# Kernel tuning notes

Measured on AMD Instinct MI355X. Metric: run time of the kernel, lower is better.

Reference implementation:

```python
import jax, jax.numpy as jnp
import numpy as np

N_NODES = 50000
N_EDGES = 800000
DIMS = [128, 512, 256, 128]
EPS = 1e-5


def setup_inputs() -> dict:
    key = jax.random.key(0)
    ks = jax.random.split(key, 2 + 5 * 3)
    inp = {
        "x": jax.random.normal(ks[0], (N_NODES, DIMS[0]), dtype=jnp.float32),
        "edge_index": jax.random.randint(ks[1], (2, N_EDGES), 0, N_NODES, dtype=jnp.int64),
    }
    ki = 2
    for i in range(3):
        din, dout = DIMS[i], DIMS[i + 1]
        s = 1.0 / np.sqrt(din)
        inp[f"Wl{i}"] = jax.random.uniform(ks[ki + 0], (din, dout), jnp.float32, -s, s)
        inp[f"bl{i}"] = jax.random.uniform(ks[ki + 1], (dout,), jnp.float32, -s, s)
        inp[f"Wr{i}"] = jax.random.uniform(ks[ki + 2], (din, dout), jnp.float32, -s, s)
        inp[f"g{i}"] = jnp.ones((dout,), jnp.float32)
        inp[f"b{i}"] = jnp.zeros((dout,), jnp.float32)
        ki += 5
    return inp


def _sage_mean(x, src, dst, Wl, bl, Wr):
    n = x.shape[0]
    agg = jax.ops.segment_sum(x[src], dst, num_segments=n)  # [N, din]
    deg = jax.ops.segment_sum(jnp.ones((src.shape[0],), x.dtype), dst, num_segments=n)
    mean = agg / jnp.maximum(deg, 1.0)[:, None]
    return mean @ Wl + bl + x @ Wr


def _bn(h, gamma, beta):
    m = h.mean(axis=0)
    v = h.var(axis=0)
    return gamma * (h - m) * jax.lax.rsqrt(v + EPS) + beta


def reference(x, edge_index, Wl0, bl0, Wr0, g0, b0, Wl1, bl1, Wr1, g1, b1, Wl2, bl2, Wr2, g2, b2):
    src, dst = edge_index[0], edge_index[1]
    params = [(Wl0, bl0, Wr0, g0, b0), (Wl1, bl1, Wr1, g1, b1), (Wl2, bl2, Wr2, g2, b2)]
    h = x
    for Wl, bl, Wr, g, b in params:
        h = _sage_mean(h, src, dst, Wl, bl, Wr)
        h = _bn(h, g, b)
        h = jax.nn.relu(h)
        # dropout: identity in eval mode
    return h
```

## Files before the change

kernel.cpp:

```cpp
#include <hip/hip_runtime.h>
#include <cstdint>
#include <cstddef>


#define EPS_BN 1e-5f

typedef unsigned short ushort_t;
typedef __attribute__((ext_vector_type(8))) short short8;
typedef __attribute__((ext_vector_type(4))) float float4v;

__device__ __forceinline__ float bf2f(ushort_t u) {
    union { unsigned int i; float f; } v; v.i = ((unsigned int)u) << 16; return v.f;
}
__device__ __forceinline__ ushort_t f2bf(float f) {
    union { float f; unsigned int i; } v; v.f = f;
    unsigned int r = v.i + 0x7fffu + ((v.i >> 16) & 1u);
    return (ushort_t)(r >> 16);
}

__device__ __forceinline__ void async_copy16(void* lds, const void* g) {
    __builtin_amdgcn_global_load_lds(
        (const __attribute__((address_space(1))) unsigned int*)g,
        (__attribute__((address_space(3))) unsigned int*)lds, 16, 0, 0);
}

__global__ void detect_fmt_kernel(const int* __restrict__ edges, int* __restrict__ nz) {
    int t = threadIdx.x;
    int cnt = 0;
    #pragma unroll
    for (int j = 0; j < 4; ++j) {
        int idx = 2 * (t * 4 + j) + 1;
        if (edges[idx] != 0) cnt++;
    }
    if (cnt) atomicAdd(nz, cnt);
}

__device__ __forceinline__ void edge_sd(const int* __restrict__ p, int e, int ne,
                                        bool is64, int& s, int& d) {
    if (is64) { s = p[2 * e];  d = p[2 * ne + 2 * e]; }
    else      { s = p[e];      d = p[ne + e]; }
}

__global__ void count_deg_kernel(const int* __restrict__ edges, int ne,
                                 const int* __restrict__ nz, int* __restrict__ degi) {
    bool is64 = (*nz == 0);
    int e = blockIdx.x * 256 + threadIdx.x;
    if (e < ne) {
        int s, d; edge_sd(edges, e, ne, is64, s, d);
        atomicAdd(&degi[d], 1);
    }
}

__global__ void scan1_kernel(const int* __restrict__ degi, int n,
                             int* __restrict__ rowptr, int* __restrict__ bsums) {
    __shared__ int sh[1024];
    int t = threadIdx.x;
    int i = blockIdx.x * 1024 + t;
    int v = (i < n) ? degi[i] : 0;
    sh[t] = v;
    __syncthreads();
    for (int off = 1; off < 1024; off <<= 1) {
        int x = (t >= off) ? sh[t - off] : 0;
        __syncthreads();
        sh[t] += x;
        __syncthreads();
    }
    if (i < n) rowptr[i] = sh[t] - v;
    if (t == 1023) bsums[blockIdx.x] = sh[t];
}

__global__ void scan2_kernel(int* __restrict__ bsums, int nb,
                             int* __restrict__ rowptr, int n, int total) {
    if (threadIdx.x == 0 && blockIdx.x == 0) {
        int run = 0;
        for (int b = 0; b < nb; ++b) { int t = bsums[b]; bsums[b] = run; run += t; }
        rowptr[n] = total;
    }
}

__global__ void scan3_kernel(int* __restrict__ rowptr, int n,
                             const int* __restrict__ bsums, int* __restrict__ cursor) {
    int i = blockIdx.x * 1024 + threadIdx.x;
    if (i < n) {
        int v = rowptr[i] + bsums[blockIdx.x];
        rowptr[i] = v;
        cursor[i] = v;
    }
}

__global__ void scatter_kernel(const int* __restrict__ edges, int ne,
                               const int* __restrict__ nz,
                               int* __restrict__ cursor, int* __restrict__ csr_src) {
    bool is64 = (*nz == 0);
    int e = blockIdx.x * 256 + threadIdx.x;
    if (e < ne) {
        int s, d; edge_sd(edges, e, ne, is64, s, d);
        int pos = atomicAdd(&cursor[d], 1);
        csr_src[pos] = s;
    }
}

__global__ void f2b_kernel(const float* __restrict__ in, ushort_t* __restrict__ out, int n) {
    int i = blockIdx.x * 256 + threadIdx.x;
    if (i < n) out[i] = f2bf(in[i]);
}

__global__ void prep_wt_kernel(const float* __restrict__ Wl, const float* __restrict__ Wr,
                               ushort_t* __restrict__ WT, int K1, int Dout) {
    int idx = blockIdx.x * 256 + threadIdx.x;
    int K2 = 2 * K1;
    if (idx >= Dout * K2) return;
    int n = idx / K2, k = idx - n * K2;
    float v = (k < K1) ? Wl[(size_t)k * Dout + n] : Wr[(size_t)(k - K1) * Dout + n];
    WT[idx] = f2bf(v);
}

__global__ void prep_wtc_kernel(const float* __restrict__ Wl, const float* __restrict__ Wr,
                                ushort_t* __restrict__ WTc, int K, int D) {
    int idx = blockIdx.x * 256 + threadIdx.x;
    if (idx >= 2 * D * K) return;
    int nn = idx / K, k = idx - nn * K;
    float v = (nn < D) ? Wl[(size_t)k * D + nn] : Wr[(size_t)k * D + (nn - D)];
    WTc[idx] = f2bf(v);
}

template <int VEC> struct VecT;
template <> struct VecT<2> { using T = unsigned int; };
template <> struct VecT<4> { using T = uint2; };
template <> struct VecT<8> { using T = uint4; };

template <int VEC>
__device__ __forceinline__ void vunpack(typename VecT<VEC>::T v, unsigned int* w) {
    if constexpr (VEC == 2) { w[0] = v; }
    else if constexpr (VEC == 4) { w[0] = v.x; w[1] = v.y; }
    else { w[0] = v.x; w[1] = v.y; w[2] = v.z; w[3] = v.w; }
}

template <int VEC>
__device__ __forceinline__ void vaccum(typename VecT<VEC>::T v, float* acc) {
    unsigned int w[VEC / 2];
    vunpack<VEC>(v, w);
    #pragma unroll
    for (int i = 0; i < VEC / 2; ++i) {
        acc[2 * i + 0] += bf2f((ushort_t)(w[i] & 0xffffu));
        acc[2 * i + 1] += bf2f((ushort_t)(w[i] >> 16));
    }
}

template <int VEC>
__global__ __launch_bounds__(256) void aggregate_wave_kernel(
    const ushort_t* __restrict__ h, ushort_t* __restrict__ mean,
    const int* __restrict__ rowptr, const int* __restrict__ csr_src, int nnodes) {
    const int din = VEC * 64;
    int wid = blockIdx.x * 4 + (threadIdx.x >> 6);
    if (wid >= nnodes) return;
    int lane = threadIdx.x & 63;
    int e0 = rowptr[wid], e1 = rowptr[wid + 1];
    const ushort_t* base = h + (size_t)lane * VEC;

    float acc[VEC];
    #pragma unroll
    for (int i = 0; i < VEC; ++i) acc[i] = 0.f;

    using VT = typename VecT<VEC>::T;
    int e = e0;
    for (; e + 4 <= e1; e += 4) {
        int s0 = csr_src[e], s1 = csr_src[e + 1], s2 = csr_src[e + 2], s3 = csr_src[e + 3];
        VT v0 = *(const VT*)(base + (size_t)s0 * din);
        VT v1 = *(const VT*)(base + (size_t)s1 * din);
        VT v2 = *(const VT*)(base + (size_t)s2 * din);
        VT v3 = *(const VT*)(base + (size_t)s3 * din);
        vaccum<VEC>(v0, acc); vaccum<VEC>(v1, acc);
        vaccum<VEC>(v2, acc); vaccum<VEC>(v3, acc);
    }
    for (; e < e1; ++e) {
        int s = csr_src[e];
        vaccum<VEC>(*(const VT*)(base + (size_t)s * din), acc);
    }

    int deg = e1 - e0;
    float scale = 1.0f / (float)(deg > 1 ? deg : 1);
    unsigned int o[VEC / 2];
    #pragma unroll
    for (int i = 0; i < VEC / 2; ++i)
        o[i] = (unsigned int)f2bf(acc[2 * i] * scale) |
               ((unsigned int)f2bf(acc[2 * i + 1] * scale) << 16);
    VT ov;
    if constexpr (VEC == 2) { ov = o[0]; }
    else if constexpr (VEC == 4) { ov.x = o[0]; ov.y = o[1]; }
    else { ov.x = o[0]; ov.y = o[1]; ov.z = o[2]; ov.w = o[3]; }
    *(VT*)(mean + (size_t)wid * din + (size_t)lane * VEC) = ov;
}

template <int VEC>
__global__ __launch_bounds__(256) void aggregate_add_kernel(
    const ushort_t* __restrict__ PR, const float* __restrict__ bias,
    float* __restrict__ outf,
    const int* __restrict__ rowptr, const int* __restrict__ csr_src, int nnodes) {
    const int D = VEC * 64;
    const int stride = 2 * D;
    int wid = blockIdx.x * 4 + (threadIdx.x >> 6);
    if (wid >= nnodes) return;
    int lane = threadIdx.x & 63;
    int e0 = rowptr[wid], e1 = rowptr[wid + 1];
    const ushort_t* base = PR + (size_t)lane * VEC;

    float acc[VEC];
    #pragma unroll
    for (int i = 0; i < VEC; ++i) acc[i] = 0.f;

    using VT = typename VecT<VEC>::T;
    int e = e0;
    for (; e + 4 <= e1; e += 4) {
        int s0 = csr_src[e], s1 = csr_src[e + 1], s2 = csr_src[e + 2], s3 = csr_src[e + 3];
        VT v0 = *(const VT*)(base + (size_t)s0 * stride);
        VT v1 = *(const VT*)(base + (size_t)s1 * stride);
        VT v2 = *(const VT*)(base + (size_t)s2 * stride);
        VT v3 = *(const VT*)(base + (size_t)s3 * stride);
        vaccum<VEC>(v0, acc); vaccum<VEC>(v1, acc);
        vaccum<VEC>(v2, acc); vaccum<VEC>(v3, acc);
    }
    for (; e < e1; ++e) {
        int s = csr_src[e];
        vaccum<VEC>(*(const VT*)(base + (size_t)s * stride), acc);
    }

    int deg = e1 - e0;
    float scale = 1.0f / (float)(deg > 1 ? deg : 1);

    VT rv = *(const VT*)(PR + (size_t)wid * stride + D + (size_t)lane * VEC);
    unsigned int rw[VEC / 2];
    vunpack<VEC>(rv, rw);
    float o[VEC];
    #pragma unroll
    for (int i = 0; i < VEC / 2; ++i) {
        o[2 * i + 0] = bf2f((ushort_t)(rw[i] & 0xffffu));
        o[2 * i + 1] = bf2f((ushort_t)(rw[i] >> 16));
    }
    #pragma unroll
    for (int i = 0; i < VEC; ++i)
        o[i] += acc[i] * scale + bias[lane * VEC + i];
    #pragma unroll
    for (int i = 0; i < VEC; ++i)
        outf[(size_t)wid * D + lane * VEC + i] = o[i];
}

template <bool DUAL, bool BF16OUT>
__global__ __launch_bounds__(256) void gemm_glds_kernel(
    const ushort_t* __restrict__ A1, const ushort_t* __restrict__ A2,
    const ushort_t* __restrict__ BT, const float* __restrict__ bias,
    float* __restrict__ Cf, ushort_t* __restrict__ Cb,
    int N, int K1, int Ktot, int Wtot) {
    __shared__ ushort_t As[128 * 32];
    __shared__ ushort_t Bs[128 * 32];

    const int tid = threadIdx.x;
    const int wave = tid >> 6;
    const int lane = tid & 63;
    const int quad = lane >> 4;
    const int l15 = lane & 15;
    const int rowBase = blockIdx.y * 128;
    const int colBase = blockIdx.x * 128;
    const int wm = (wave >> 1) * 64;
    const int wn = (wave & 1) * 64;

    float4v acc[4][4];
    #pragma unroll
    for (int i = 0; i < 4; ++i)
        #pragma unroll
        for (int j = 0; j < 4; ++j)
            acc[i][j] = (float4v){0.f, 0.f, 0.f, 0.f};

    const int nkt = Ktot / 32;
    const int khalf = K1 / 32;

    for (int kt = 0; kt < nkt; ++kt) {
        const ushort_t* Asrc = A1;
        int kg = kt * 32;
        if (DUAL && kt >= khalf) { Asrc = A2; kg = (kt - khalf) * 32; }
        const int kb = kt * 32;

        #pragma unroll
        for (int u = 0; u < 2; ++u) {
            int c = u * 256 + tid;
            int r = c >> 2, off = (c & 3) * 8;
            int grow = rowBase + r;
            if (grow >= N) grow = N - 1;
            async_copy16(&As[c * 8], Asrc + (size_t)grow * K1 + kg + off);
            async_copy16(&Bs[c * 8], BT + (size_t)(colBase + r) * Ktot + kb + off);
        }
        __syncthreads();

        short8 af[4], bf4[4];
        #pragma unroll
        for (int i = 0; i < 4; ++i)
            af[i] = *(const short8*)&As[(wm + i * 16 + l15) * 32 + quad * 8];
        #pragma unroll
        for (int j = 0; j < 4; ++j)
            bf4[j] = *(const short8*)&Bs[(wn + j * 16 + l15) * 32 + quad * 8];

        #pragma unroll
        for (int i = 0; i < 4; ++i)
            #pragma unroll
            for (int j = 0; j < 4; ++j)
                acc[i][j] = __builtin_amdgcn_mfma_f32_16x16x32_bf16(bf4[j], af[i], acc[i][j], 0, 0, 0);
        __syncthreads();
    }

    if (BF16OUT) {
        ushort_t* lws = (wave < 2) ? &As[wave * 2048] : &Bs[(wave - 2) * 2048];
        #pragma unroll
        for (int p = 0; p < 2; ++p) {
            #pragma unroll
            for (int jj = 0; jj < 2; ++jj) {
                int j = 2 * p + jj;
                #pragma unroll
                for (int i = 0; i < 4; ++i) {
                    uint2 pk;
                    pk.x = (unsigned int)f2bf(acc[i][j][0]) | ((unsigned int)f2bf(acc[i][j][1]) << 16);
                    pk.y = (unsigned int)f2bf(acc[i][j][2]) | ((unsigned int)f2bf(acc[i][j][3]) << 16);
                    *(uint2*)&lws[(i * 16 + l15) * 32 + jj * 16 + quad * 4] = pk;
                }
            }
            __syncthreads();
            #pragma unroll
            for (int it = 0; it < 4; ++it) {
                int c = it * 64 + lane;
                int row = c >> 2, coff = (c & 3) * 8;
                int grow = rowBase + wm + row;
                if (grow < N) {
                    uint4 v = *(const uint4*)&lws[row * 32 + coff];
                    *(uint4*)(Cb + (size_t)grow * Wtot + colBase + wn + p * 32 + coff) = v;
                }
            }
            __syncthreads();
        }
    } else {
        float* lwf = (float*)((wave < 2) ? (void*)&As[wave * 2048] : (void*)&Bs[(wave - 2) * 2048]);
        #pragma unroll
        for (int j = 0; j < 4; ++j) {
            int colb = colBase + wn + j * 16 + quad * 4;
            float4 bv = *(const float4*)(bias + colb);
            #pragma unroll
            for (int i = 0; i < 4; ++i) {
                float4 o;
                o.x = acc[i][j][0] + bv.x;
                o.y = acc[i][j][1] + bv.y;
                o.z = acc[i][j][2] + bv.z;
                o.w = acc[i][j][3] + bv.w;
                *(float4*)&lwf[(i * 16 + l15) * 16 + quad * 4] = o;
            }
            __syncthreads();
            #pragma unroll
            for (int it = 0; it < 4; ++it) {
                int c = it * 64 + lane;
                int row = c >> 2, coff = (c & 3) * 4;
                int grow = rowBase + wm + row;
                if (grow < N)
                    *(float4*)(Cf + (size_t)grow * Wtot + colBase + wn + j * 16 + coff) =
                        *(const float4*)&lwf[row * 16 + coff];
            }
            __syncthreads();
        }
    }
}

__global__ void colstats_kernel(const float* __restrict__ h, int N, int D,
                                float* __restrict__ sum, float* __restrict__ sumsq) {
    int col = blockIdx.x * 64 + (threadIdx.x & 63);
    int lane = threadIdx.x >> 6;
    float s = 0.f, s2 = 0.f;
    int stride = gridDim.y * 4;
    for (int r = blockIdx.y * 4 + lane; r < N; r += stride) {
        float v = h[(size_t)r * D + col];
        s += v;
        s2 += v * v;
    }
    atomicAdd(&sum[col], s);
    atomicAdd(&sumsq[col], s2);
}

__global__ void bn_relu_bf16_kernel(const float* __restrict__ h, ushort_t* __restrict__ hb,
                                    int N, int D,
                                    const float* __restrict__ sum, const float* __restrict__ sumsq,
                                    const float* __restrict__ g, const float* __restrict__ b) {
    size_t idx = (size_t)blockIdx.x * blockDim.x + threadIdx.x;
    if (idx >= (size_t)N * D) return;
    int col = (int)(idx & (size_t)(D - 1));
    float m = sum[col] / (float)N;
    float var = sumsq[col] / (float)N - m * m;
    float inv = rsqrtf(var + EPS_BN);
    float v = h[idx];
    v = g[col] * (v - m) * inv + b[col];
    hb[idx] = f2bf(v > 0.f ? v : 0.f);
}

__global__ void bn_relu_kernel(float* __restrict__ h, int N, int D,
                               const float* __restrict__ sum, const float* __restrict__ sumsq,
                               const float* __restrict__ g, const float* __restrict__ b) {
    size_t idx = (size_t)blockIdx.x * blockDim.x + threadIdx.x;
    if (idx >= (size_t)N * D) return;
    int col = (int)(idx & (size_t)(D - 1));
    float m = sum[col] / (float)N;
    float var = sumsq[col] / (float)N - m * m;
    float inv = rsqrtf(var + EPS_BN);
    float v = h[idx];
    v = g[col] * (v - m) * inv + b[col];
    h[idx] = v > 0.f ? v : 0.f;
}

extern "C" void kernel_launch(void* const* d_in, const int* in_sizes, int n_in,
                              void* d_out, int out_size, void* d_ws, size_t ws_size,
                              hipStream_t stream) {
    const float* x     = (const float*)d_in[0];
    const int*   edges = (const int*)d_in[1];
    const float* Wl0 = (const float*)d_in[2];
    const float* bl0 = (const float*)d_in[3];
    const float* Wr0 = (const float*)d_in[4];
    const float* g0  = (const float*)d_in[5];
    const float* b0  = (const float*)d_in[6];
    const float* Wl1 = (const float*)d_in[7];
    const float* bl1 = (const float*)d_in[8];
    const float* Wr1 = (const float*)d_in[9];
    const float* g1  = (const float*)d_in[10];
    const float* b1  = (const float*)d_in[11];
    const float* Wl2 = (const float*)d_in[12];
    const float* bl2 = (const float*)d_in[13];
    const float* Wr2 = (const float*)d_in[14];
    const float* g2  = (const float*)d_in[15];
    const float* b2  = (const float*)d_in[16];

    const int D0 = 128, D1 = 512, D2 = 256, D3 = 128;
    const int n  = in_sizes[0] / D0;
    const int ne = in_sizes[1] / 2;

    char* base = (char*)d_ws;
    size_t off = 0;
    auto alloc = [&](size_t bytes) -> char* {
        char* p = base + off;
        off = (off + bytes + 255) & ~(size_t)255;
        return p;
    };
    int*      nzflag  = (int*)alloc(4);
    int*      degi    = (int*)alloc((size_t)n * 4);
    int*      rowptr  = (int*)alloc((size_t)(n + 1) * 4);
    int*      cursor  = (int*)alloc((size_t)n * 4);
    int*      csr_src = (int*)alloc((size_t)ne * 4);
    int*      bsums   = (int*)alloc(64 * 4);
    float*    stats   = (float*)alloc(6 * 512 * 4);
    ushort_t* xb      = (ushort_t*)alloc((size_t)n * D0 * 2);
    ushort_t* mb      = (ushort_t*)alloc((size_t)n * 512 * 2);
    ushort_t* h1b     = (ushort_t*)alloc((size_t)n * D1 * 2);
    ushort_t* h2b     = (ushort_t*)alloc((size_t)n * D2 * 2);
    float*    hf      = (float*)alloc((size_t)n * 512 * 4);
    ushort_t* WT0     = (ushort_t*)alloc((size_t)D1 * 2 * D0 * 2);
    ushort_t* WT1c    = (ushort_t*)alloc((size_t)(2 * D2) * D1 * 2);
    ushort_t* WT2c    = (ushort_t*)alloc((size_t)(2 * D3) * D2 * 2);
    float*    out     = (float*)d_out;
    (void)ws_size; (void)n_in; (void)out_size;

    hipMemsetAsync(nzflag, 0, 4, stream);
    hipMemsetAsync(degi, 0, (size_t)n * 4, stream);
    hipMemsetAsync(stats, 0, 6 * 512 * 4, stream);

    detect_fmt_kernel<<<1, 256, 0, stream>>>(edges, nzflag);
    count_deg_kernel<<<(ne + 255) / 256, 256, 0, stream>>>(edges, ne, nzflag, degi);
    int nscan = (n + 1023) / 1024;
    scan1_kernel<<<nscan, 1024, 0, stream>>>(degi, n, rowptr, bsums);
    scan2_kernel<<<1, 64, 0, stream>>>(bsums, nscan, rowptr, n, ne);
    scan3_kernel<<<nscan, 1024, 0, stream>>>(rowptr, n, bsums, cursor);
    scatter_kernel<<<(ne + 255) / 256, 256, 0, stream>>>(edges, ne, nzflag, cursor, csr_src);

    f2b_kernel<<<((size_t)n * D0 + 255) / 256, 256, 0, stream>>>(x, xb, n * D0);
    prep_wt_kernel<<<(D1 * 2 * D0 + 255) / 256, 256, 0, stream>>>(Wl0, Wr0, WT0, D0, D1);
    prep_wtc_kernel<<<(2 * D2 * D1 + 255) / 256, 256, 0, stream>>>(Wl1, Wr1, WT1c, D1, D2);
    prep_wtc_kernel<<<(2 * D3 * D2 + 255) / 256, 256, 0, stream>>>(Wl2, Wr2, WT2c, D2, D3);

    const int aggGrid = (n + 3) / 4;
    const int rowBlocks = (n + 127) / 128;

    aggregate_wave_kernel<2><<<aggGrid, 256, 0, stream>>>(xb, mb, rowptr, csr_src, n);
    gemm_glds_kernel<true, false><<<dim3(D1 / 128, rowBlocks), 256, 0, stream>>>(
        mb, xb, WT0, bl0, hf, nullptr, n, D0, 2 * D0, D1);
    colstats_kernel<<<dim3(D1 / 64, 128), 256, 0, stream>>>(hf, n, D1, stats + 0 * 1024, stats + 0 * 1024 + 512);
    bn_relu_bf16_kernel<<<((size_t)n * D1 + 255) / 256, 256, 0, stream>>>(
        hf, h1b, n, D1, stats + 0 * 1024, stats + 0 * 1024 + 512, g0, b0);

    gemm_glds_kernel<false, true><<<dim3(2 * D2 / 128, rowBlocks), 256, 0, stream>>>(
        h1b, nullptr, WT1c, nullptr, nullptr, mb, n, D1, D1, 2 * D2);
    aggregate_add_kernel<4><<<aggGrid, 256, 0, stream>>>(
        mb, bl1, hf, rowptr, csr_src, n);
    colstats_kernel<<<dim3(D2 / 64, 128), 256, 0, stream>>>(hf, n, D2, stats + 1 * 1024, stats + 1 * 1024 + 512);
    bn_relu_bf16_kernel<<<((size_t)n * D2 + 255) / 256, 256, 0, stream>>>(
        hf, h2b, n, D2, stats + 1 * 1024, stats + 1 * 1024 + 512, g1, b1);

    gemm_glds_kernel<false, true><<<dim3(2 * D3 / 128, rowBlocks), 256, 0, stream>>>(
        h2b, nullptr, WT2c, nullptr, nullptr, mb, n, D2, D2, 2 * D3);
    aggregate_add_kernel<2><<<aggGrid, 256, 0, stream>>>(
        mb, bl2, out, rowptr, csr_src, n);
    colstats_kernel<<<dim3(D3 / 64, 128), 256, 0, stream>>>(out, n, D3, stats + 2 * 1024, stats + 2 * 1024 + 512);
    bn_relu_kernel<<<((size_t)n * D3 + 255) / 256, 256, 0, stream>>>(
        out, n, D3, stats + 2 * 1024, stats + 2 * 1024 + 512, g2, b2);
}
```

Measured before the change: 674.1 us.

## Store pre-BN activations as bf16 and unroll gather loop to eight edges

Pre-batchnorm activations from the GEMM and aggregate-add kernels are now written as bf16 instead of fp32. The column-stats and BN+ReLU kernels are rewritten to read bf16 and process two columns per thread. The edge gather loop is factored into a helper that keeps eight loads in flight. This halves the memory traffic of the stats and normalisation passes, at the cost of bf16 rounding of pre-normalisation values before the statistics are computed.

```diff
diff --git a/kernel.cpp b/kernel.cpp
--- a/kernel.cpp
+++ b/kernel.cpp
@@ -148,6 +148,39 @@
 }
 
 template <int VEC>
+__device__ __forceinline__ void gather_sum(
+    const ushort_t* __restrict__ base, const int* __restrict__ csr_src,
+    int e0, int e1, int rstride, float* acc) {
+    using VT = typename VecT<VEC>::T;
+    int e = e0;
+    for (; e + 8 <= e1; e += 8) {
+        VT v[8];
+        #pragma unroll
+        for (int u = 0; u < 8; ++u)
+            v[u] = *(const VT*)(base + (size_t)csr_src[e + u] * rstride);
+        #pragma unroll
+        for (int u = 0; u < 8; ++u) vaccum<VEC>(v[u], acc);
+    }
+    if (e + 4 <= e1) {
+        VT v[4];
+        #pragma unroll
+        for (int u = 0; u < 4; ++u)
+            v[u] = *(const VT*)(base + (size_t)csr_src[e + u] * rstride);
+        #pragma unroll
+        for (int u = 0; u < 4; ++u) vaccum<VEC>(v[u], acc);
+        e += 4;
+    }
+    if (e + 2 <= e1) {
+        VT v0 = *(const VT*)(base + (size_t)csr_src[e] * rstride);
+        VT v1 = *(const VT*)(base + (size_t)csr_src[e + 1] * rstride);
+        vaccum<VEC>(v0, acc); vaccum<VEC>(v1, acc);
+        e += 2;
+    }
+    if (e < e1)
+        vaccum<VEC>(*(const VT*)(base + (size_t)csr_src[e] * rstride), acc);
+}
+
+template <int VEC>
 __global__ __launch_bounds__(256) void aggregate_wave_kernel(
     const ushort_t* __restrict__ h, ushort_t* __restrict__ mean,
     const int* __restrict__ rowptr, const int* __restrict__ csr_src, int nnodes) {
@@ -156,27 +189,11 @@
     if (wid >= nnodes) return;
     int lane = threadIdx.x & 63;
     int e0 = rowptr[wid], e1 = rowptr[wid + 1];
-    const ushort_t* base = h + (size_t)lane * VEC;
 
     float acc[VEC];
     #pragma unroll
     for (int i = 0; i < VEC; ++i) acc[i] = 0.f;
-
-    using VT = typename VecT<VEC>::T;
-    int e = e0;
-    for (; e + 4 <= e1; e += 4) {
-        int s0 = csr_src[e], s1 = csr_src[e + 1], s2 = csr_src[e + 2], s3 = csr_src[e + 3];
-        VT v0 = *(const VT*)(base + (size_t)s0 * din);
-        VT v1 = *(const VT*)(base + (size_t)s1 * din);
-        VT v2 = *(const VT*)(base + (size_t)s2 * din);
-        VT v3 = *(const VT*)(base + (size_t)s3 * din);
-        vaccum<VEC>(v0, acc); vaccum<VEC>(v1, acc);
-        vaccum<VEC>(v2, acc); vaccum<VEC>(v3, acc);
-    }
-    for (; e < e1; ++e) {
-        int s = csr_src[e];
-        vaccum<VEC>(*(const VT*)(base + (size_t)s * din), acc);
-    }
+    gather_sum<VEC>(h + (size_t)lane * VEC, csr_src, e0, e1, din, acc);
 
     int deg = e1 - e0;
     float scale = 1.0f / (float)(deg > 1 ? deg : 1);
@@ -185,6 +202,7 @@
     for (int i = 0; i < VEC / 2; ++i)
         o[i] = (unsigned int)f2bf(acc[2 * i] * scale) |
                ((unsigned int)f2bf(acc[2 * i + 1] * scale) << 16);
+    using VT = typename VecT<VEC>::T;
     VT ov;
     if constexpr (VEC == 2) { ov = o[0]; }
     else if constexpr (VEC == 4) { ov.x = o[0]; ov.y = o[1]; }
@@ -195,7 +213,7 @@
 template <int VEC>
 __global__ __launch_bounds__(256) void aggregate_add_kernel(
     const ushort_t* __restrict__ PR, const float* __restrict__ bias,
-    float* __restrict__ outf,
+    ushort_t* __restrict__ pre,
     const int* __restrict__ rowptr, const int* __restrict__ csr_src, int nnodes) {
     const int D = VEC * 64;
     const int stride = 2 * D;
@@ -203,31 +221,16 @@
     if (wid >= nnodes) return;
     int lane = threadIdx.x & 63;
     int e0 = rowptr[wid], e1 = rowptr[wid + 1];
-    const ushort_t* base = PR + (size_t)lane * VEC;
 
     float acc[VEC];
     #pragma unroll
     for (int i = 0; i < VEC; ++i) acc[i] = 0.f;
-
-    using VT = typename VecT<VEC>::T;
-    int e = e0;
-    for (; e + 4 <= e1; e += 4) {
-        int s0 = csr_src[e], s1 = csr_src[e + 1], s2 = csr_src[e + 2], s3 = csr_src[e + 3];
-        VT v0 = *(const VT*)(base + (size_t)s0 * stride);
-        VT v1 = *(const VT*)(base + (size_t)s1 * stride);
-        VT v2 = *(const VT*)(base + (size_t)s2 * stride);
-        VT v3 = *(const VT*)(base + (size_t)s3 * stride);
-        vaccum<VEC>(v0, acc); vaccum<VEC>(v1, acc);
-        vaccum<VEC>(v2, acc); vaccum<VEC>(v3, acc);
-    }
-    for (; e < e1; ++e) {
-        int s = csr_src[e];
-        vaccum<VEC>(*(const VT*)(base + (size_t)s * stride), acc);
-    }
+    gather_sum<VEC>(PR + (size_t)lane * VEC, csr_src, e0, e1, stride, acc);
 
     int deg = e1 - e0;
     float scale = 1.0f / (float)(deg > 1 ? deg : 1);
 
+    using VT = typename VecT<VEC>::T;
     VT rv = *(const VT*)(PR + (size_t)wid * stride + D + (size_t)lane * VEC);
     unsigned int rw[VEC / 2];
     vunpack<VEC>(rv, rw);
@@ -240,17 +243,23 @@
     #pragma unroll
     for (int i = 0; i < VEC; ++i)
         o[i] += acc[i] * scale + bias[lane * VEC + i];
-    #pragma unroll
-    for (int i = 0; i < VEC; ++i)
-        outf[(size_t)wid * D + lane * VEC + i] = o[i];
-}
-
-template <bool DUAL, bool BF16OUT>
+
+    unsigned int ow[VEC / 2];
+    #pragma unroll
+    for (int i = 0; i < VEC / 2; ++i)
+        ow[i] = (unsigned int)f2bf(o[2 * i]) | ((unsigned int)f2bf(o[2 * i + 1]) << 16);
+    VT ov;
+    if constexpr (VEC == 2) { ov = ow[0]; }
+    else if constexpr (VEC == 4) { ov.x = ow[0]; ov.y = ow[1]; }
+    else { ov.x = ow[0]; ov.y = ow[1]; ov.z = ow[2]; ov.w = ow[3]; }
+    *(VT*)(pre + (size_t)wid * D + (size_t)lane * VEC) = ov;
+}
+
+template <bool DUAL, bool BIAS>
 __global__ __launch_bounds__(256) void gemm_glds_kernel(
     const ushort_t* __restrict__ A1, const ushort_t* __restrict__ A2,
     const ushort_t* __restrict__ BT, const float* __restrict__ bias,
-    float* __restrict__ Cf, ushort_t* __restrict__ Cb,
-    int N, int K1, int Ktot, int Wtot) {
+    ushort_t* __restrict__ Cb, int N, int K1, int Ktot, int Wtot) {
     __shared__ ushort_t As[128 * 32];
     __shared__ ushort_t Bs[128 * 32];
 
@@ -307,106 +316,97 @@
         __syncthreads();
     }
 
-    if (BF16OUT) {
-        ushort_t* lws = (wave < 2) ? &As[wave * 2048] : &Bs[(wave - 2) * 2048];
-        #pragma unroll
-        for (int p = 0; p < 2; ++p) {
-            #pragma unroll
-            for (int jj = 0; jj < 2; ++jj) {
-                int j = 2 * p + jj;
-                #pragma unroll
-                for (int i = 0; i < 4; ++i) {
-                    uint2 pk;
-                    pk.x = (unsigned int)f2bf(acc[i][j][0]) | ((unsigned int)f2bf(acc[i][j][1]) << 16);
-                    pk.y = (unsigned int)f2bf(acc[i][j][2]) | ((unsigned int)f2bf(acc[i][j][3]) << 16);
-                    *(uint2*)&lws[(i * 16 + l15) * 32 + jj * 16 + quad * 4] = pk;
-                }
-            }
-            __syncthreads();
-            #pragma unroll
-            for (int it = 0; it < 4; ++it) {
-                int c = it * 64 + lane;
-                int row = c >> 2, coff = (c & 3) * 8;
-                int grow = rowBase + wm + row;
-                if (grow < N) {
-                    uint4 v = *(const uint4*)&lws[row * 32 + coff];
-                    *(uint4*)(Cb + (size_t)grow * Wtot + colBase + wn + p * 32 + coff) = v;
-                }
-            }
-            __syncthreads();
-        }
-    } else {
-        float* lwf = (float*)((wave < 2) ? (void*)&As[wave * 2048] : (void*)&Bs[(wave - 2) * 2048]);
-        #pragma unroll
-        for (int j = 0; j < 4; ++j) {
-            int colb = colBase + wn + j * 16 + quad * 4;
-            float4 bv = *(const float4*)(bias + colb);
+    ushort_t* lws = (wave < 2) ? &As[wave * 2048] : &Bs[(wave - 2) * 2048];
+    #pragma unroll
+    for (int p = 0; p < 2; ++p) {
+        #pragma unroll
+        for (int jj = 0; jj < 2; ++jj) {
+            int j = 2 * p + jj;
+            float4 bv = make_float4(0.f, 0.f, 0.f, 0.f);
+            if (BIAS) bv = *(const float4*)(bias + colBase + wn + j * 16 + quad * 4);
             #pragma unroll
             for (int i = 0; i < 4; ++i) {
-                float4 o;
-                o.x = acc[i][j][0] + bv.x;
-                o.y = acc[i][j][1] + bv.y;
-                o.z = acc[i][j][2] + bv.z;
-                o.w = acc[i][j][3] + bv.w;
-                *(float4*)&lwf[(i * 16 + l15) * 16 + quad * 4] = o;
+                uint2 pk;
+                pk.x = (unsigned int)f2bf(acc[i][j][0] + bv.x) |
+                       ((unsigned int)f2bf(acc[i][j][1] + bv.y) << 16);
+                pk.y = (unsigned int)f2bf(acc[i][j][2] + bv.z) |
+                       ((unsigned int)f2bf(acc[i][j][3] + bv.w) << 16);
+                *(uint2*)&lws[(i * 16 + l15) * 32 + jj * 16 + quad * 4] = pk;
             }
-            __syncthreads();
-            #pragma unroll
-            for (int it = 0; it < 4; ++it) {
-                int c = it * 64 + lane;
-                int row = c >> 2, coff = (c & 3) * 4;
-                int grow = rowBase + wm + row;
-                if (grow < N)
-                    *(float4*)(Cf + (size_t)grow * Wtot + colBase + wn + j * 16 + coff) =
-                        *(const float4*)&lwf[row * 16 + coff];
+        }
+        __syncthreads();
+        #pragma unroll
+        for (int it = 0; it < 4; ++it) {
+            int c = it * 64 + lane;
+            int row = c >> 2, coff = (c & 3) * 8;
+            int grow = rowBase + wm + row;
+            if (grow < N) {
+                uint4 v = *(const uint4*)&lws[row * 32 + coff];
+                *(uint4*)(Cb + (size_t)grow * Wtot + colBase + wn + p * 32 + coff) = v;
             }
-            __syncthreads();
         }
-    }
-}
-
-__global__ void colstats_kernel(const float* __restrict__ h, int N, int D,
-                                float* __restrict__ sum, float* __restrict__ sumsq) {
-    int col = blockIdx.x * 64 + (threadIdx.x & 63);
-    int lane = threadIdx.x >> 6;
-    float s = 0.f, s2 = 0.f;
+        __syncthreads();
+    }
+}
+
+__global__ void colstats_b_kernel(const ushort_t* __restrict__ h, int N, int D,
+                                  float* __restrict__ sum, float* __restrict__ sumsq) {
+    int c2 = blockIdx.x * 128 + (threadIdx.x & 63) * 2;
+    int rl = threadIdx.x >> 6;
+    float s0 = 0.f, s20 = 0.f, s1 = 0.f, s21 = 0.f;
     int stride = gridDim.y * 4;
-    for (int r = blockIdx.y * 4 + lane; r < N; r += stride) {
-        float v = h[(size_t)r * D + col];
-        s += v;
-        s2 += v * v;
-    }
-    atomicAdd(&sum[col], s);
-    atomicAdd(&sumsq[col], s2);
-}
-
-__global__ void bn_relu_bf16_kernel(const float* __restrict__ h, ushort_t* __restrict__ hb,
-                                    int N, int D,
-                                    const float* __restrict__ sum, const float* __restrict__ sumsq,
-                                    const float* __restrict__ g, const float* __restrict__ b) {
+    for (int r = blockIdx.y * 4 + rl; r < N; r += stride) {
+        unsigned int w = *(const unsigned int*)(h + (size_t)r * D + c2);
+        float v0 = bf2f((ushort_t)(w & 0xffffu));
+        float v1 = bf2f((ushort_t)(w >> 16));
+        s0 += v0; s20 += v0 * v0;
+        s1 += v1; s21 += v1 * v1;
+    }
+    atomicAdd(&sum[c2 + 0], s0);
+    atomicAdd(&sumsq[c2 + 0], s20);
+    atomicAdd(&sum[c2 + 1], s1);
+    atomicAdd(&sumsq[c2 + 1], s21);
+}
+
+__global__ void bn_relu_b2b_kernel(const ushort_t* __restrict__ h, ushort_t* __restrict__ hb,
+                                   int N, int D,
+                                   const float* __restrict__ sum, const float* __restrict__ sumsq,
+                                   const float* __restrict__ g, const float* __restrict__ b) {
     size_t idx = (size_t)blockIdx.x * blockDim.x + threadIdx.x;
-    if (idx >= (size_t)N * D) return;
-    int col = (int)(idx & (size_t)(D - 1));
-    float m = sum[col] / (float)N;
-    float var = sumsq[col] / (float)N - m * m;
-    float inv = rsqrtf(var + EPS_BN);
-    float v = h[idx];
-    v = g[col] * (v - m) * inv + b[col];
-    hb[idx] = f2bf(v > 0.f ? v : 0.f);
-}
-
-__global__ void bn_relu_kernel(float* __restrict__ h, int N, int D,
-                               const float* __restrict__ sum, const float* __restrict__ sumsq,
-                               const float* __restrict__ g, const float* __restrict__ b) {
+    size_t tot = (size_t)N * D / 2;
+    if (idx >= tot) return;
+    int cp = (int)(idx & (size_t)(D / 2 - 1));
+    int c0 = cp * 2, c1 = c0 + 1;
+    float m0 = sum[c0] / (float)N, m1 = sum[c1] / (float)N;
+    float i0 = rsqrtf(sumsq[c0] / (float)N - m0 * m0 + EPS_BN);
+    float i1 = rsqrtf(sumsq[c1] / (float)N - m1 * m1 + EPS_BN);
+    unsigned int w = ((const unsigned int*)h)[idx];
+    float v0 = g[c0] * (bf2f((ushort_t)(w & 0xffffu)) - m0) * i0 + b[c0];
+    float v1 = g[c1] * (bf2f((ushort_t)(w >> 16)) - m1) * i1 + b[c1];
+    v0 = v0 > 0.f ? v0 : 0.f;
+    v1 = v1 > 0.f ? v1 : 0.f;
+    ((unsigned int*)hb)[idx] = (unsigned int)f2bf(v0) | ((unsigned int)f2bf(v1) << 16);
+}
+
+__global__ void bn_relu_b2f_kernel(const ushort_t* __restrict__ h, float* __restrict__ hf,
+                                   int N, int D,
+                                   const float* __restrict__ sum, const float* __restrict__ sumsq,
+                                   const float* __restrict__ g, const float* __restrict__ b) {
     size_t idx = (size_t)blockIdx.x * blockDim.x + threadIdx.x;
-    if (idx >= (size_t)N * D) return;
-    int col = (int)(idx & (size_t)(D - 1));
-    float m = sum[col] / (float)N;
-    float var = sumsq[col] / (float)N - m * m;
-    float inv = rsqrtf(var + EPS_BN);
-    float v = h[idx];
-    v = g[col] * (v - m) * inv + b[col];
-    h[idx] = v > 0.f ? v : 0.f;
+    size_t tot = (size_t)N * D / 2;
+    if (idx >= tot) return;
+    int cp = (int)(idx & (size_t)(D / 2 - 1));
+    int c0 = cp * 2, c1 = c0 + 1;
+    float m0 = sum[c0] / (float)N, m1 = sum[c1] / (float)N;
+    float i0 = rsqrtf(sumsq[c0] / (float)N - m0 * m0 + EPS_BN);
+    float i1 = rsqrtf(sumsq[c1] / (float)N - m1 * m1 + EPS_BN);
+    unsigned int w = ((const unsigned int*)h)[idx];
+    float v0 = g[c0] * (bf2f((ushort_t)(w & 0xffffu)) - m0) * i0 + b[c0];
+    float v1 = g[c1] * (bf2f((ushort_t)(w >> 16)) - m1) * i1 + b[c1];
+    float2 o;
+    o.x = v0 > 0.f ? v0 : 0.f;
+    o.y = v1 > 0.f ? v1 : 0.f;
+    *(float2*)(hf + idx * 2) = o;
 }
 
 extern "C" void kernel_launch(void* const* d_in, const int* in_sizes, int n_in,
@@ -452,7 +452,7 @@
     ushort_t* mb      = (ushort_t*)alloc((size_t)n * 512 * 2);
     ushort_t* h1b     = (ushort_t*)alloc((size_t)n * D1 * 2);
     ushort_t* h2b     = (ushort_t*)alloc((size_t)n * D2 * 2);
-    float*    hf      = (float*)alloc((size_t)n * 512 * 4);
+    ushort_t* hpre    = (ushort_t*)alloc((size_t)n * 512 * 2);
     ushort_t* WT0     = (ushort_t*)alloc((size_t)D1 * 2 * D0 * 2);
     ushort_t* WT1c    = (ushort_t*)alloc((size_t)(2 * D2) * D1 * 2);
     ushort_t* WT2c    = (ushort_t*)alloc((size_t)(2 * D3) * D2 * 2);
@@ -478,27 +478,30 @@
 
     const int aggGrid = (n + 3) / 4;
     const int rowBlocks = (n + 127) / 128;
+    float* st0 = stats + 0 * 1024;
+    float* st1 = stats + 1 * 1024;
+    float* st2 = stats + 2 * 1024;
 
     aggregate_wave_kernel<2><<<aggGrid, 256, 0, stream>>>(xb, mb, rowptr, csr_src, n);
-    gemm_glds_kernel<true, false><<<dim3(D1 / 128, rowBlocks), 256, 0, stream>>>(
-        mb, xb, WT0, bl0, hf, nullptr, n, D0, 2 * D0, D1);
-    colstats_kernel<<<dim3(D1 / 64, 128), 256, 0, stream>>>(hf, n, D1, stats + 0 * 1024, stats + 0 * 1024 + 512);
-    bn_relu_bf16_kernel<<<((size_t)n * D1 + 255) / 256, 256, 0, stream>>>(
-        hf, h1b, n, D1, stats + 0 * 1024, stats + 0 * 1024 + 512, g0, b0);
-
-    gemm_glds_kernel<false, true><<<dim3(2 * D2 / 128, rowBlocks), 256, 0, stream>>>(
-        h1b, nullptr, WT1c, nullptr, nullptr, mb, n, D1, D1, 2 * D2);
+    gemm_glds_kernel<true, true><<<dim3(D1 / 128, rowBlocks), 256, 0, stream>>>(
+        mb, xb, WT0, bl0, hpre, n, D0, 2 * D0, D1);
+    colstats_b_kernel<<<dim3(D1 / 128, 128), 256, 0, stream>>>(hpre, n, D1, st0, st0 + 512);
+    bn_relu_b2b_kernel<<<((size_t)n * D1 / 2 + 255) / 256, 256, 0, stream>>>(
+        hpre, h1b, n, D1, st0, st0 + 512, g0, b0);
+
+    gemm_glds_kernel<false, false><<<dim3(2 * D2 / 128, rowBlocks), 256, 0, stream>>>(
+        h1b, nullptr, WT1c, nullptr, mb, n, D1, D1, 2 * D2);
     aggregate_add_kernel<4><<<aggGrid, 256, 0, stream>>>(
-        mb, bl1, hf, rowptr, csr_src, n);
-    colstats_kernel<<<dim3(D2 / 64, 128), 256, 0, stream>>>(hf, n, D2, stats + 1 * 1024, stats + 1 * 1024 + 512);
-    bn_relu_bf16_kernel<<<((size_t)n * D2 + 255) / 256, 256, 0, stream>>>(
-        hf, h2b, n, D2, stats + 1 * 1024, stats + 1 * 1024 + 512, g1, b1);
-
-    gemm_glds_kernel<false, true><<<dim3(2 * D3 / 128, rowBlocks), 256, 0, stream>>>(
-        h2b, nullptr, WT2c, nullptr, nullptr, mb, n, D2, D2, 2 * D3);
+        mb, bl1, hpre, rowptr, csr_src, n);
+    colstats_b_kernel<<<dim3(D2 / 128, 128), 256, 0, stream>>>(hpre, n, D2, st1, st1 + 512);
+    bn_relu_b2b_kernel<<<((size_t)n * D2 / 2 + 255) / 256, 256, 0, stream>>>(
+        hpre, h2b, n, D2, st1, st1 + 512, g1, b1);
+
+    gemm_glds_kernel<false, false><<<dim3(2 * D3 / 128, rowBlocks), 256, 0, stream>>>(
+        h2b, nullptr, WT2c, nullptr, mb, n, D2, D2, 2 * D3);
     aggregate_add_kernel<2><<<aggGrid, 256, 0, stream>>>(
-        mb, bl2, out, rowptr, csr_src, n);
-    colstats_kernel<<<dim3(D3 / 64, 128), 256, 0, stream>>>(out, n, D3, stats + 2 * 1024, stats + 2 * 1024 + 512);
-    bn_relu_kernel<<<((size_t)n * D3 + 255) / 256, 256, 0, stream>>>(
-        out, n, D3, stats + 2 * 1024, stats + 2 * 1024 + 512, g2, b2);
-}
+        mb, bl2, hpre, rowptr, csr_src, n);
+    colstats_b_kernel<<<dim3(D3 / 128, 128), 256, 0, stream>>>(hpre, n, D3, st2, st2 + 512);
+    bn_relu_b2f_kernel<<<((size_t)n * D3 / 2 + 255) / 256, 256, 0, stream>>>(
+        hpre, out, n, D3, st2, st2 + 512, g2, b2);
+}
```

Result: no change. 665.1 us (-1.3%).
